# Optimization experiments

Hardware: AMD Instinct MI355X
Metric: run time of the kernel (lower is better)

## Reference

```python
import jax, jax.numpy as jnp
import numpy as np

MASS, CHARGE, ALPHA, BETA = 1.0, 0.5, 0.1, 0.05
ETA = jnp.array([1.0, -1.0, -1.0, -1.0], dtype=jnp.float32)  # Minkowski metric diag


def setup_inputs() -> dict:
    key = jax.random.key(0)
    k1, k2, k3 = jax.random.split(key, 3)
    B = 262144
    y = jax.random.normal(k1, (B, 8), dtype=jnp.float32)
    W = jax.random.normal(k2, (4, 4), dtype=jnp.float32) * 0.3
    V = jax.random.normal(k3, (4, 4), dtype=jnp.float32) * 0.3
    return {"y": y, "W": W, "V": V}


def _lagrangian(z):
    # z = (x, u, A) concatenated, shape [12]
    x, u, A = z[0:4], z[4:8], z[8:12]
    kinetic = 0.5 * MASS * jnp.sum(ETA * u * u)
    coupling = CHARGE * jnp.sum(ETA * u * A)
    xu_term = ALPHA * jnp.sum((x * u) ** 2)      # makes J_xu nontrivial
    uA_term = BETA * jnp.sum(u * A) ** 2          # makes J_Au nontrivial
    return kinetic + coupling + xu_term + uA_term


def reference(y, W, V):
    def A_vec(x):  # vector potential A^mu(x), works on [4] or [B,4]
        return jnp.tanh(x @ W.T) + x @ V.T

    x = y[:, 0:4]   # [B,4] positions
    u = y[:, 4:8]   # [B,4] velocities
    A = A_vec(x)    # [B,4]
    z = jnp.concatenate([x, u, A], axis=1)  # [B,12] = (x,u,A)

    gradL = jax.vmap(jax.grad(_lagrangian))(z)      # [B,12]
    H = jax.vmap(jax.hessian(_lagrangian))(z)       # [B,12,12]

    dL_dx = gradL[:, 0:4]
    dL_dA = gradL[:, 8:12]
    J_xu = H[:, 0:4, 4:8]    # d^2L/(dx^mu du^nu)
    J_uu = H[:, 4:8, 4:8]    # d^2L/(du^mu du^nu)
    J_Au = H[:, 8:12, 4:8]   # d^2L/(dA^mu du^nu)

    # dA_dx[a, nu, i] = dA^i/dx^nu (matches tf.stack(..., axis=2) layout)
    jacA = jax.vmap(jax.jacfwd(A_vec))(x)           # [B, i, nu]
    dA_dx = jnp.transpose(jacA, (0, 2, 1))          # [B, nu, i]

    J_uu_inv = jnp.linalg.pinv(J_uu)                # [B,4,4]

    force = (dL_dx
             + jnp.einsum('ajk,ak->aj', dA_dx, dL_dA)
             - jnp.einsum('ai,aij->aj', u,
                          J_xu + jnp.einsum('ajk,akm->ajm', dA_dx, J_Au)))
    acceleration = jnp.einsum('ai,aij->aj', force, J_uu_inv)  # [B,4]
    return acceleration
```

## Files before the change

kernel.cpp:

```cpp
#include <hip/hip_runtime.h>
#include <math.h>


#define SIX_RCOND 2.86102294921875e-5
#define RCOND     4.76837158203125e-6

__device__ __forceinline__ float rcp_nr(float x) {
    float r = __builtin_amdgcn_rcpf(x);
    r = r * (2.0f - x * r);
    return r;
}

__device__ __forceinline__ void fast_tanh4(const double t[4], double th[4])
{
    const double LOG2E = 1.4426950408889634074;
    const double LN2HI = 6.93147180369123816490e-01;
    const double LN2LO = 1.90821492927058770002e-10;
    double e[4], opp[4];
    #pragma unroll
    for (int j = 0; j < 4; ++j) {
        double a  = fabs(t[j]);
        double z  = -2.0 * a;
        double zc = fmax(z, -64.0);
        double nf = rint(zc * LOG2E);
        double r  = fma(-nf, LN2HI, zc);
        r = fma(-nf, LN2LO, r);
        double p = 2.75573192239858906526e-07;
        p = fma(p, r, 2.75573192239858925110e-06);
        p = fma(p, r, 2.48015873015873015873e-05);
        p = fma(p, r, 1.98412698412698412698e-04);
        p = fma(p, r, 1.38888888888888888889e-03);
        p = fma(p, r, 8.33333333333333333333e-03);
        p = fma(p, r, 4.16666666666666666667e-02);
        p = fma(p, r, 1.66666666666666666667e-01);
        p = fma(p, r, 0.5);
        p = fma(p, r, 1.0);
        p = fma(p, r, 1.0);
        int n = (int)nf;
        double twon = __longlong_as_double(((long long)(1023 + n)) << 52);
        double ez = p * twon;
        ez = (z <= -40.0) ? 0.0 : ez;
        e[j]   = ez;
        opp[j] = 1.0 + ez;
    }
    double p01 = opp[0] * opp[1], p23 = opp[2] * opp[3];
    double rp  = 1.0 / (p01 * p23);
    double inv[4] = { opp[1] * p23 * rp, opp[0] * p23 * rp,
                      p01 * opp[3] * rp, p01 * opp[2] * rp };
    #pragma unroll
    for (int j = 0; j < 4; ++j)
        th[j] = copysign((1.0 - e[j]) * inv[j], t[j]);
}

__device__ __forceinline__ void model_terms_f64(
    const double* sW, const double* sV,
    const double x[4], const double u[4],
    double A[4], double f[4], double d[4])
{
    const double eta[4] = {1.0, -1.0, -1.0, -1.0};
    const double CHG = 0.5, ALPHA = 0.1, BETA = 0.05;
    double t[4], s[4];
    #pragma unroll
    for (int j = 0; j < 4; ++j) {
        double tj = 0.0, sj = 0.0;
        #pragma unroll
        for (int k = 0; k < 4; ++k) {
            tj = fma(sW[j*4+k], x[k], tj);
            sj = fma(sV[j*4+k], x[k], sj);
        }
        t[j] = tj; s[j] = sj;
    }
    double th[4];
    fast_tanh4(t, th);
    double G[4][4];
    #pragma unroll
    for (int j = 0; j < 4; ++j) {
        A[j] = th[j] + s[j];
        double dth = 1.0 - th[j] * th[j];
        #pragma unroll
        for (int k = 0; k < 4; ++k) G[j][k] = fma(dth, sW[j*4+k], sV[j*4+k]);
    }
    double S = 0.0;
    #pragma unroll
    for (int k = 0; k < 4; ++k) S += u[k] * A[k];
    double P[4], R[4], Q[4];
    #pragma unroll
    for (int j = 0; j < 4; ++j) {
        double p = 0.0, r = 0.0, q = 0.0;
        #pragma unroll
        for (int k = 0; k < 4; ++k) {
            p += G[k][j] * u[k];
            r += G[j][k] * u[k];
            q += G[k][j] * (CHG * eta[k]) * u[k];
        }
        P[j] = p; R[j] = r; Q[j] = q;
    }
    double T = 0.0;
    #pragma unroll
    for (int j = 0; j < 4; ++j) T += u[j] * R[j];
    #pragma unroll
    for (int j = 0; j < 4; ++j) {
        f[j] = -2.0 * ALPHA * x[j] * u[j] * u[j]
             + Q[j]
             + 2.0 * BETA * S * P[j]
             - (CHG * eta[j] + 2.0 * BETA * S) * R[j]
             - 2.0 * BETA * A[j] * T;
        d[j] = eta[j] + 2.0 * ALPHA * x[j] * x[j];
    }
}

__device__ __forceinline__ void sm_solve_f64(
    const double d[4], const double A[4], const double f[4], double acc[4])
{
    const double C2 = 0.1;
    double b[4], fd[4], den = 1.0, w = 0.0;
    #pragma unroll
    for (int j = 0; j < 4; ++j) {
        double inv = 1.0 / d[j];
        b[j]  = A[j] * inv;
        fd[j] = f[j] * inv;
        den  += C2 * A[j] * b[j];
        w    += b[j] * f[j];
    }
    double scale = C2 * w / den;
    #pragma unroll
    for (int j = 0; j < 4; ++j) acc[j] = fd[j] - b[j] * scale;
}

__device__ __forceinline__ bool criterion_f64(
    const double d[4], const double A[4])
{
    const double C2 = 0.1;
    double mind = 1e300;
    #pragma unroll
    for (int j = 0; j < 4; ++j) {
        double a = fabs(d[j]);
        mind = (a < mind) ? a : mind;
    }
    double p01 = d[0] * d[1], p23 = d[2] * d[3];
    double det = p01 * p23
        + C2 * (A[0]*A[0]*(d[1]*p23) + A[1]*A[1]*(d[0]*p23) +
                A[2]*A[2]*(p01*d[3]) + A[3]*A[3]*(p01*d[2]));
    double sumA2 = 0.0, sumA4 = 0.0, F2 = 0.0;
    #pragma unroll
    for (int j = 0; j < 4; ++j) {
        double Aj2 = A[j] * A[j];
        sumA2 += Aj2; sumA4 += Aj2 * Aj2;
        double Jjj = d[j] + C2 * Aj2;
        F2 += Jjj * Jjj;
    }
    F2 += C2 * C2 * (sumA2 * sumA2 - sumA4);
    double rowmax = 0.0;
    #pragma unroll
    for (int r = 0; r < 4; ++r) {
        double rs = 0.0;
        #pragma unroll
        for (int c = 0; c < 4; ++c) {
            double Jrc = C2 * A[r] * A[c] + ((r == c) ? d[r] : 0.0);
            rs += fabs(Jrc);
        }
        rowmax = (rs > rowmax) ? rs : rowmax;
    }
    double sig_hi2 = rowmax * rowmax;
    sig_hi2 = (F2 < sig_hi2) ? F2 : sig_hi2;
    return (fabs(det) > SIX_RCOND * sig_hi2 * sig_hi2) && (mind > 1e-3);
}

__device__ __forceinline__ void jacobi_pinv_lds(
    const double d[4], const double A[4], const double f[4], double acc[4],
    double* __restrict__ Vm)
{
    const double C2 = 0.1;
    double M[4][4];
    #pragma unroll
    for (int r = 0; r < 4; ++r) {
        #pragma unroll
        for (int c = 0; c < 4; ++c) {
            M[r][c] = C2 * A[r] * A[c];
            Vm[r*4+c] = (r == c) ? 1.0 : 0.0;
        }
        M[r][r] += d[r];
    }
    for (int sweep = 0; sweep < 8; ++sweep) {
        #pragma unroll
        for (int p = 0; p < 3; ++p) {
            #pragma unroll
            for (int q2 = p + 1; q2 < 4; ++q2) {
                double apq = M[p][q2];
                bool active = fabs(apq) > 1e-280;
                double div = active ? (2.0 * apq) : 1.0;
                double tau = (M[q2][q2] - M[p][p]) / div;
                double tt = ((tau >= 0.0) ? 1.0 : -1.0) /
                            (fabs(tau) + sqrt(1.0 + tau * tau));
                double c = 1.0 / sqrt(1.0 + tt * tt);
                double s = tt * c;
                c = active ? c : 1.0;
                s = active ? s : 0.0;
                #pragma unroll
                for (int k = 0; k < 4; ++k) {
                    double mkp = M[k][p], mkq = M[k][q2];
                    M[k][p]  = c * mkp - s * mkq;
                    M[k][q2] = s * mkp + c * mkq;
                }
                #pragma unroll
                for (int k = 0; k < 4; ++k) {
                    double mpk = M[p][k], mqk = M[q2][k];
                    M[p][k]  = c * mpk - s * mqk;
                    M[q2][k] = s * mpk + c * mqk;
                }
                #pragma unroll
                for (int k = 0; k < 4; ++k) {
                    double vkp = Vm[k*4+p], vkq = Vm[k*4+q2];
                    Vm[k*4+p]  = c * vkp - s * vkq;
                    Vm[k*4+q2] = s * vkp + c * vkq;
                }
            }
        }
    }
    double lam[4], sigmax = 0.0;
    #pragma unroll
    for (int k = 0; k < 4; ++k) {
        lam[k] = M[k][k];
        double a = fabs(lam[k]);
        sigmax = (a > sigmax) ? a : sigmax;
    }
    double cutoff = RCOND * sigmax;
    #pragma unroll
    for (int j = 0; j < 4; ++j) acc[j] = 0.0;
    #pragma unroll
    for (int e = 0; e < 4; ++e) {
        double coef = 0.0;
        #pragma unroll
        for (int k = 0; k < 4; ++k) coef += Vm[k*4+e] * f[k];
        coef /= lam[e];
        coef = (fabs(lam[e]) > cutoff) ? coef : 0.0;
        #pragma unroll
        for (int j = 0; j < 4; ++j) acc[j] += coef * Vm[j*4+e];
    }
}

__global__ __launch_bounds__(256) void fast_kernel(
    const float* __restrict__ y, const float* __restrict__ W,
    const float* __restrict__ V, float* __restrict__ out,
    unsigned int* __restrict__ cnt, int* __restrict__ list,
    unsigned int cap, int B)
{
    __shared__ float  sW[16],  sV[16];
    __shared__ double sWd[16], sVd[16];
    if (threadIdx.x < 16) {
        float w = W[threadIdx.x];
        sW[threadIdx.x]  = w;
        sWd[threadIdx.x] = (double)w;
    } else if (threadIdx.x < 32) {
        float v = V[threadIdx.x - 16];
        sV[threadIdx.x - 16]  = v;
        sVd[threadIdx.x - 16] = (double)v;
    }
    __syncthreads();

    int i = blockIdx.x * blockDim.x + threadIdx.x;
    if (i >= B) return;

    const float4* y4 = (const float4*)y;
    float4 xv = y4[2 * i];
    float4 uv = y4[2 * i + 1];
    float x[4] = {xv.x, xv.y, xv.z, xv.w};
    float u[4] = {uv.x, uv.y, uv.z, uv.w};

    const float eta[4] = {1.0f, -1.0f, -1.0f, -1.0f};
    const float CHG = 0.5f, ALPHA = 0.1f, BETA = 0.05f, C2 = 0.1f;
    const float NEG2LOG2E = -2.8853900817779268f;

    float t[4], sv[4];
    #pragma unroll
    for (int j = 0; j < 4; ++j) {
        float tj = 0.0f, sj = 0.0f;
        #pragma unroll
        for (int k = 0; k < 4; ++k) {
            tj = fmaf(sW[j*4+k], x[k], tj);
            sj = fmaf(sV[j*4+k], x[k], sj);
        }
        t[j] = tj; sv[j] = sj;
    }
    float A[4], dth[4];
    #pragma unroll
    for (int j = 0; j < 4; ++j) {
        float a  = fabsf(t[j]);
        float e  = __builtin_amdgcn_exp2f(a * NEG2LOG2E);
        float th = copysignf((1.0f - e) * rcp_nr(1.0f + e), t[j]);
        A[j]   = th + sv[j];
        dth[j] = 1.0f - th * th;
    }
    float G[4][4];
    #pragma unroll
    for (int j = 0; j < 4; ++j)
        #pragma unroll
        for (int k = 0; k < 4; ++k)
            G[j][k] = fmaf(dth[j], sW[j*4+k], sV[j*4+k]);

    float S = 0.0f;
    #pragma unroll
    for (int k = 0; k < 4; ++k) S = fmaf(u[k], A[k], S);
    float P[4], R[4], Q[4];
    #pragma unroll
    for (int j = 0; j < 4; ++j) {
        float p = 0.0f, r = 0.0f, q = 0.0f;
        #pragma unroll
        for (int k = 0; k < 4; ++k) {
            p = fmaf(G[k][j], u[k], p);
            r = fmaf(G[j][k], u[k], r);
            q = fmaf(G[k][j] * (CHG * eta[k]), u[k], q);
        }
        P[j] = p; R[j] = r; Q[j] = q;
    }
    float T = 0.0f;
    #pragma unroll
    for (int j = 0; j < 4; ++j) T = fmaf(u[j], R[j], T);
    float f[4], d[4];
    #pragma unroll
    for (int j = 0; j < 4; ++j) {
        f[j] = -2.0f * ALPHA * x[j] * u[j] * u[j]
             + Q[j]
             + 2.0f * BETA * S * P[j]
             - (CHG * eta[j] + 2.0f * BETA * S) * R[j]
             - 2.0f * BETA * A[j] * T;
        d[j] = eta[j] + 2.0f * ALPHA * x[j] * x[j];
    }

    float mind = fminf(fminf(fabsf(d[0]), fabsf(d[1])),
                       fminf(fabsf(d[2]), fabsf(d[3])));
    float p01 = d[0] * d[1], p23 = d[2] * d[3];
    float prod = p01 * p23;
    float det = prod
        + C2 * (A[0]*A[0]*(d[1]*p23) + A[1]*A[1]*(d[0]*p23) +
                A[2]*A[2]*(p01*d[3]) + A[3]*A[3]*(p01*d[2]));
    float rowmax = 0.0f;
    #pragma unroll
    for (int r = 0; r < 4; ++r) {
        float rs = 0.0f;
        #pragma unroll
        for (int c = 0; c < 4; ++c) {
            float Jrc = C2 * A[r] * A[c] + ((r == c) ? d[r] : 0.0f);
            rs += fabsf(Jrc);
        }
        rowmax = fmaxf(rs, rowmax);
    }
    float sig2 = rowmax * rowmax;
    bool safe = (fabsf(det) > sig2 * sig2 * (1.0f / 1024.0f)) && (mind > 1e-3f);

    if (safe) {
        float invprod = rcp_nr(prod);
        float invd[4] = { d[1] * p23 * invprod, d[0] * p23 * invprod,
                          p01 * d[3] * invprod, p01 * d[2] * invprod };
        float b[4], fd[4], den = 1.0f, w = 0.0f;
        #pragma unroll
        for (int j = 0; j < 4; ++j) {
            b[j]  = A[j] * invd[j];
            fd[j] = f[j] * invd[j];
            den   = fmaf(C2 * A[j], b[j], den);
            w     = fmaf(b[j], f[j], w);
        }
        float scale = (C2 * w) * rcp_nr(den);
        float4 res;
        res.x = fd[0] - b[0] * scale; res.y = fd[1] - b[1] * scale;
        res.z = fd[2] - b[2] * scale; res.w = fd[3] - b[3] * scale;
        ((float4*)out)[i] = res;
    } else {
        double xd[4] = {xv.x, xv.y, xv.z, xv.w};
        double ud[4] = {uv.x, uv.y, uv.z, uv.w};
        double Ad[4], fd64[4], dd[4];
        model_terms_f64(sWd, sVd, xd, ud, Ad, fd64, dd);
        bool safe64 = criterion_f64(dd, Ad);
        bool deferred = false;
        if (!safe64) {
            unsigned int idx = atomicAdd(cnt, 1u);
            if (idx < cap) { list[idx] = i; deferred = true; }
        }
        if (!deferred) {
            double acc[4];
            sm_solve_f64(dd, Ad, fd64, acc);
            float4 res;
            res.x = (float)acc[0]; res.y = (float)acc[1];
            res.z = (float)acc[2]; res.w = (float)acc[3];
            ((float4*)out)[i] = res;
        }
    }
}

__global__ __launch_bounds__(64, 1) void slow_kernel(
    const float* __restrict__ y, const float* __restrict__ W,
    const float* __restrict__ V, float* __restrict__ out,
    const unsigned int* __restrict__ cnt, const int* __restrict__ list,
    unsigned int cap)
{
    __shared__ double sW[16], sV[16];
    __shared__ double VmL[64][17];
    if (threadIdx.x < 16)      sW[threadIdx.x]      = (double)W[threadIdx.x];
    else if (threadIdx.x < 32) sV[threadIdx.x - 16] = (double)V[threadIdx.x - 16];
    __syncthreads();

    unsigned int n = *cnt;
    if (n > cap) n = cap;
    int stride = gridDim.x * blockDim.x;
    for (unsigned int j = blockIdx.x * blockDim.x + threadIdx.x; j < n; j += stride) {
        int i = list[j];
        const float4* y4 = (const float4*)y;
        float4 xv = y4[2 * i];
        float4 uv = y4[2 * i + 1];
        double x[4] = {xv.x, xv.y, xv.z, xv.w};
        double u[4] = {uv.x, uv.y, uv.z, uv.w};
        double A[4], f[4], d[4];
        model_terms_f64(sW, sV, x, u, A, f, d);

        double acc[4];
        jacobi_pinv_lds(d, A, f, acc, VmL[threadIdx.x]);

        float4 res;
        res.x = (float)acc[0]; res.y = (float)acc[1];
        res.z = (float)acc[2]; res.w = (float)acc[3];
        ((float4*)out)[i] = res;
    }
}

extern "C" void kernel_launch(void* const* d_in, const int* in_sizes, int n_in,
                              void* d_out, int out_size, void* d_ws, size_t ws_size,
                              hipStream_t stream) {
    const float* y = (const float*)d_in[0];
    const float* W = (const float*)d_in[1];
    const float* V = (const float*)d_in[2];
    float* out = (float*)d_out;
    int B = in_sizes[0] / 8;

    unsigned int* cnt = (unsigned int*)d_ws;
    int* list = (int*)((char*)d_ws + 16);
    unsigned int cap = (ws_size > 16) ? (unsigned int)((ws_size - 16) / sizeof(int)) : 0u;
    if (cap > (unsigned int)B) cap = (unsigned int)B;

    hipMemsetAsync(d_ws, 0, 16, stream);

    int block = 256;
    int grid = (B + block - 1) / block;
    fast_kernel<<<grid, block, 0, stream>>>(y, W, V, out, cnt, list, cap, B);
    slow_kernel<<<256, 64, 0, stream>>>(y, W, V, out, cnt, list, cap);
}
```

Measured before the change: 83.88 us.

## Split f64 fallback path out of fast kernel into separate mid-tier kernel

The fast kernel no longer computes the double-precision model terms inline for unsafe rows. It appends them to a first worklist, which a new mid kernel processes in f64, deferring the hardest cases to a second list for the Jacobi slow kernel. Dropping the f64 code and shared double arrays from the fast kernel should cut its register pressure and raise occupancy. The cost is an extra kernel launch, more atomics, and a halved worklist capacity. If the first list overflows, the fast kernel falls back to an unchecked f32 solve.

```diff
diff --git a/kernel.cpp b/kernel.cpp
--- a/kernel.cpp
+++ b/kernel.cpp
@@ -242,20 +242,12 @@
 __global__ __launch_bounds__(256) void fast_kernel(
     const float* __restrict__ y, const float* __restrict__ W,
     const float* __restrict__ V, float* __restrict__ out,
-    unsigned int* __restrict__ cnt, int* __restrict__ list,
-    unsigned int cap, int B)
-{
-    __shared__ float  sW[16],  sV[16];
-    __shared__ double sWd[16], sVd[16];
-    if (threadIdx.x < 16) {
-        float w = W[threadIdx.x];
-        sW[threadIdx.x]  = w;
-        sWd[threadIdx.x] = (double)w;
-    } else if (threadIdx.x < 32) {
-        float v = V[threadIdx.x - 16];
-        sV[threadIdx.x - 16]  = v;
-        sVd[threadIdx.x - 16] = (double)v;
-    }
+    unsigned int* __restrict__ cnt1, int* __restrict__ list1,
+    unsigned int cap1, int B)
+{
+    __shared__ float sW[16], sV[16];
+    if (threadIdx.x < 16)      sW[threadIdx.x]      = W[threadIdx.x];
+    else if (threadIdx.x < 32) sV[threadIdx.x - 16] = V[threadIdx.x - 16];
     __syncthreads();
 
     int i = blockIdx.x * blockDim.x + threadIdx.x;
@@ -366,19 +358,63 @@
         res.z = fd[2] - b[2] * scale; res.w = fd[3] - b[3] * scale;
         ((float4*)out)[i] = res;
     } else {
-        double xd[4] = {xv.x, xv.y, xv.z, xv.w};
-        double ud[4] = {uv.x, uv.y, uv.z, uv.w};
-        double Ad[4], fd64[4], dd[4];
-        model_terms_f64(sWd, sVd, xd, ud, Ad, fd64, dd);
-        bool safe64 = criterion_f64(dd, Ad);
+        unsigned int idx = atomicAdd(cnt1, 1u);
+        if (idx < cap1) {
+            list1[idx] = i;
+        } else {
+            float b[4], fd[4], den = 1.0f, w = 0.0f;
+            #pragma unroll
+            for (int j = 0; j < 4; ++j) {
+                float inv = rcp_nr(d[j]);
+                b[j]  = A[j] * inv;
+                fd[j] = f[j] * inv;
+                den   = fmaf(C2 * A[j], b[j], den);
+                w     = fmaf(b[j], f[j], w);
+            }
+            float scale = (C2 * w) * rcp_nr(den);
+            float4 res;
+            res.x = fd[0] - b[0] * scale; res.y = fd[1] - b[1] * scale;
+            res.z = fd[2] - b[2] * scale; res.w = fd[3] - b[3] * scale;
+            ((float4*)out)[i] = res;
+        }
+    }
+}
+
+__global__ __launch_bounds__(64, 1) void mid_kernel(
+    const float* __restrict__ y, const float* __restrict__ W,
+    const float* __restrict__ V, float* __restrict__ out,
+    const unsigned int* __restrict__ cnt1, const int* __restrict__ list1,
+    unsigned int cap1,
+    unsigned int* __restrict__ cnt2, int* __restrict__ list2,
+    unsigned int cap2)
+{
+    __shared__ double sW[16], sV[16];
+    if (threadIdx.x < 16)      sW[threadIdx.x]      = (double)W[threadIdx.x];
+    else if (threadIdx.x < 32) sV[threadIdx.x - 16] = (double)V[threadIdx.x - 16];
+    __syncthreads();
+
+    unsigned int n = *cnt1;
+    if (n > cap1) n = cap1;
+    int stride = gridDim.x * blockDim.x;
+    for (unsigned int j = blockIdx.x * blockDim.x + threadIdx.x; j < n; j += stride) {
+        int i = list1[j];
+        const float4* y4 = (const float4*)y;
+        float4 xv = y4[2 * i];
+        float4 uv = y4[2 * i + 1];
+        double x[4] = {xv.x, xv.y, xv.z, xv.w};
+        double u[4] = {uv.x, uv.y, uv.z, uv.w};
+        double A[4], f[4], d[4];
+        model_terms_f64(sW, sV, x, u, A, f, d);
+
+        bool safe64 = criterion_f64(d, A);
         bool deferred = false;
         if (!safe64) {
-            unsigned int idx = atomicAdd(cnt, 1u);
-            if (idx < cap) { list[idx] = i; deferred = true; }
+            unsigned int idx = atomicAdd(cnt2, 1u);
+            if (idx < cap2) { list2[idx] = i; deferred = true; }
         }
         if (!deferred) {
             double acc[4];
-            sm_solve_f64(dd, Ad, fd64, acc);
+            sm_solve_f64(d, A, f, acc);
             float4 res;
             res.x = (float)acc[0]; res.y = (float)acc[1];
             res.z = (float)acc[2]; res.w = (float)acc[3];
@@ -390,8 +426,8 @@
 __global__ __launch_bounds__(64, 1) void slow_kernel(
     const float* __restrict__ y, const float* __restrict__ W,
     const float* __restrict__ V, float* __restrict__ out,
-    const unsigned int* __restrict__ cnt, const int* __restrict__ list,
-    unsigned int cap)
+    const unsigned int* __restrict__ cnt2, const int* __restrict__ list2,
+    unsigned int cap2)
 {
     __shared__ double sW[16], sV[16];
     __shared__ double VmL[64][17];
@@ -399,11 +435,11 @@
     else if (threadIdx.x < 32) sV[threadIdx.x - 16] = (double)V[threadIdx.x - 16];
     __syncthreads();
 
-    unsigned int n = *cnt;
-    if (n > cap) n = cap;
+    unsigned int n = *cnt2;
+    if (n > cap2) n = cap2;
     int stride = gridDim.x * blockDim.x;
     for (unsigned int j = blockIdx.x * blockDim.x + threadIdx.x; j < n; j += stride) {
-        int i = list[j];
+        int i = list2[j];
         const float4* y4 = (const float4*)y;
         float4 xv = y4[2 * i];
         float4 uv = y4[2 * i + 1];
@@ -431,15 +467,22 @@
     float* out = (float*)d_out;
     int B = in_sizes[0] / 8;
 
-    unsigned int* cnt = (unsigned int*)d_ws;
-    int* list = (int*)((char*)d_ws + 16);
-    unsigned int cap = (ws_size > 16) ? (unsigned int)((ws_size - 16) / sizeof(int)) : 0u;
-    if (cap > (unsigned int)B) cap = (unsigned int)B;
+    unsigned int* cnt1 = (unsigned int*)d_ws;
+    unsigned int* cnt2 = cnt1 + 1;
+    unsigned int avail = (ws_size > 16) ? (unsigned int)((ws_size - 16) / sizeof(int)) : 0u;
+    unsigned int cap1 = avail / 2;
+    unsigned int cap2 = avail - cap1;
+    if (cap1 > (unsigned int)B) cap1 = (unsigned int)B;
+    if (cap2 > (unsigned int)B) cap2 = (unsigned int)B;
+    int* list1 = (int*)((char*)d_ws + 16);
+    int* list2 = list1 + cap1;
 
     hipMemsetAsync(d_ws, 0, 16, stream);
 
     int block = 256;
     int grid = (B + block - 1) / block;
-    fast_kernel<<<grid, block, 0, stream>>>(y, W, V, out, cnt, list, cap, B);
-    slow_kernel<<<256, 64, 0, stream>>>(y, W, V, out, cnt, list, cap);
-}
+    fast_kernel<<<grid, block, 0, stream>>>(y, W, V, out, cnt1, list1, cap1, B);
+    mid_kernel<<<1024, 64, 0, stream>>>(y, W, V, out, cnt1, list1, cap1,
+                                        cnt2, list2, cap2);
+    slow_kernel<<<256, 64, 0, stream>>>(y, W, V, out, cnt2, list2, cap2);
+}
```

Result: slower. 96.65 us (+15.2%).
